# Optimization experiments

Hardware: AMD Instinct MI355X
Metric: run time of the kernel (lower is better)

The kernel has to match this reference:

```python
import jax, jax.numpy as jnp
import numpy as np

B, T, E = 4, 2048, 1024
N, P = 16, 64  # num_heads, projection_dim = E // N
SCALE = P ** 0.5


def setup_inputs() -> dict:
    key = jax.random.key(0)
    k1, k2, k3 = jax.random.split(key, 3)
    x = jax.random.normal(k1, (B, T, E), dtype=jnp.float32)
    w_qkv = jax.random.normal(k2, (E, N, 3 * P), dtype=jnp.float32) * 0.02
    b_qkv = jnp.zeros((N, 3 * P), dtype=jnp.float32)
    w_o = jax.random.normal(k3, (P, N, E), dtype=jnp.float32) * 0.02
    b_o = jnp.zeros((E,), dtype=jnp.float32)
    return {"x": x, "w_qkv": w_qkv, "b_qkv": b_qkv, "w_o": w_o, "b_o": b_o}


def reference(x, w_qkv, b_qkv, w_o, b_o):
    # QKV projection: bte,enp->btnp (+ bias over n,p)
    qkv = jnp.einsum('bte,enp->btnp', x, w_qkv) + b_qkv  # [B,T,N,3P]
    qkv = jnp.transpose(qkv, (0, 2, 1, 3))               # [B,N,T,3P]
    q, k, v = jnp.split(qkv, 3, axis=-1)                 # each [B,N,T,P]
    scores = jnp.einsum('bnip,bnjp->bnij', q, k) / SCALE # [B,N,T,T]
    attn = jax.nn.softmax(scores, axis=-1)
    weighted = jnp.einsum('bnij,bnjp->bnip', attn, v)    # [B,N,T,P]
    # Output projection: bntp,pne->bte (+ bias over e)
    out = jnp.einsum('bntp,pne->bte', weighted, w_o) + b_o
    return out
```

## Files before the change

### kernel.cpp

```cpp
#include <hip/hip_runtime.h>

typedef __attribute__((ext_vector_type(8))) short bf16x8;
typedef __attribute__((ext_vector_type(4))) short s16x4;
typedef __attribute__((ext_vector_type(4))) float f32x4;
typedef __attribute__((ext_vector_type(16))) float f32x16;
typedef __attribute__((ext_vector_type(2))) unsigned u32x2;

#define MFMA16(a,b,c) __builtin_amdgcn_mfma_f32_16x16x32_bf16((a),(b),(c),0,0,0)
#define MFMA32(a,b,c) __builtin_amdgcn_mfma_f32_32x32x16_bf16((a),(b),(c),0,0,0)

static constexpr int Bsz = 4, T = 2048, E = 1024, NH = 16, HP = 64;
static constexpr int J3 = NH * 3 * HP;

__device__ __forceinline__ short f2bf(float f) {
  union { float f; unsigned u; } v; v.f = f;
  unsigned r = (v.u + 0x7fffu + ((v.u >> 16) & 1u)) >> 16;
  return (short)r;
}

__device__ __forceinline__ unsigned cvtpk(float a, float b) {
  unsigned r;
  asm("v_cvt_pk_bf16_f32 %0, %1, %2" : "=v"(r) : "v"(a), "v"(b));
  return r;
}

typedef __attribute__((address_space(3))) unsigned int lds_u32;
typedef __attribute__((address_space(1))) const unsigned int glb_u32;
__device__ __forceinline__ void gl16(const short* g, const short* l) {
  __builtin_amdgcn_global_load_lds((glb_u32*)g, (lds_u32*)l, 16, 0, 0);
}

__global__ void cvt_all(const float* __restrict__ x, s16x4* __restrict__ xb,
                        const float* __restrict__ wqkv, short* __restrict__ wqkvT,
                        const float* __restrict__ wo, short* __restrict__ woT) {
  __shared__ float tile[32][33];
  const int b = blockIdx.x;
  if (b < 8192) {
    int i = b * 256 + threadIdx.x;
    float4 v = ((const float4*)x)[i];
    s16x4 r;
    r[0] = f2bf(v.x); r[1] = f2bf(v.y); r[2] = f2bf(v.z); r[3] = f2bf(v.w);
    xb[i] = r;
  } else if (b < 11264) {
    const int bw = b - 8192;
    const int jb = (bw % 96) * 32, eb = (bw / 96) * 32;
    const int tx = threadIdx.x & 31, ty = threadIdx.x >> 5;
    for (int r = 0; r < 32; r += 8)
      tile[ty + r][tx] = wqkv[(size_t)(eb + ty + r) * J3 + jb + tx];
    __syncthreads();
    for (int r = 0; r < 32; r += 8)
      wqkvT[(size_t)(jb + ty + r) * E + eb + tx] = f2bf(tile[tx][ty + r]);
  } else {
    const int o = (b - 11264) * 256 + threadIdx.x;
    const int e = o >> 10, k = o & 1023;
    const int n = k >> 6, p = k & 63;
    woT[o] = f2bf(wo[(size_t)(p * 16 + n) * E + e]);
  }
}

__global__ __launch_bounds__(256) void gemm_qkv(
    const short* __restrict__ A,
    const short* __restrict__ Bt,
    const float* __restrict__ bias,
    short* __restrict__ Qb, short* __restrict__ Kb, short* __restrict__ Vt) {
  __shared__ short SH[17408];
  short* As = SH;
  short* Bs = SH + 8192;
  const int m0 = blockIdx.x * 128, n0 = blockIdx.y * 128;
  const int tid = threadIdx.x;
  const int lane = tid & 63, w = tid >> 6;
  const int wm = (w >> 1) * 64, wn = (w & 1) * 64;
  const int l15 = lane & 15, lh = lane >> 4;
  const int l7 = l15 & 7;

  const int rA = lane >> 3;
  const int cS = 8 * ((lane & 7) ^ rA);
  const short* Ap = A + (size_t)(m0 + w * 32 + rA) * 1024 + cS;
  const short* Bp = Bt + (size_t)(n0 + w * 32 + rA) * 1024 + cS;
  const short* AsBase = As + w * 2048;
  const short* BsBase = Bs + w * 2048;

  f32x4 acc[4][4] = {};

  for (int k0 = 0; k0 < 1024; k0 += 64) {
    __syncthreads();
#pragma unroll
    for (int j = 0; j < 4; j++) {
      gl16(Ap + j * 8192 + k0, AsBase + j * 512);
      gl16(Bp + j * 8192 + k0, BsBase + j * 512);
    }
    __syncthreads();
    bf16x8 af[2][4], bfr[2][4];
#pragma unroll
    for (int kk = 0; kk < 2; kk++) {
#pragma unroll
      for (int m = 0; m < 4; m++)
        af[kk][m] = *(const bf16x8*)(As + (wm + m * 16 + l15) * 64 + 8 * ((kk * 4 + lh) ^ l7));
#pragma unroll
      for (int n = 0; n < 4; n++)
        bfr[kk][n] = *(const bf16x8*)(Bs + (wn + n * 16 + l15) * 64 + 8 * ((kk * 4 + lh) ^ l7));
    }
#pragma unroll
    for (int m = 0; m < 4; m++)
#pragma unroll
      for (int n = 0; n < 4; n++) {
        acc[m][n] = MFMA16(af[0][m], bfr[0][n], acc[m][n]);
        acc[m][n] = MFMA16(af[1][m], bfr[1][n], acc[m][n]);
      }
  }

  const int bb = m0 >> 11, m0t = m0 & 2047;
  const int g = w & 1;
  const int jg = n0 + g * 64;
  const int nhg = jg / 192;
  const int cg = jg - nhg * 192;
  const int tyg = cg >> 6;

  __syncthreads();
  if (tyg == 2) {
    short* Vl = SH + g * 8704;
#pragma unroll
    for (int nn = 0; nn < 4; nn++) {
      const int p = nn * 16 + l15;
      const float bv = bias[jg + p];
#pragma unroll
      for (int mm = 0; mm < 4; mm++) {
        const int tok0 = wm + mm * 16 + lh * 4;
        u32x2 pk;
        pk[0] = cvtpk(acc[mm][nn][0] + bv, acc[mm][nn][1] + bv);
        pk[1] = cvtpk(acc[mm][nn][2] + bv, acc[mm][nn][3] + bv);
        *(u32x2*)(Vl + p * 136 + tok0) = pk;
      }
    }
  } else {
    const float sc = (tyg == 0) ? 0.180336880f : 1.0f;
    short* qkbase = ((tyg == 0) ? Qb : Kb) +
                    ((((size_t)(bb * 16 + nhg)) * 2048 + m0t) << 6);
#pragma unroll
    for (int nn = 0; nn < 4; nn++) {
      const int p = nn * 16 + l15;
      const float bv = bias[jg + p];
#pragma unroll
      for (int mm = 0; mm < 4; mm++) {
#pragma unroll
        for (int r = 0; r < 4; r++) {
          const int tok = wm + mm * 16 + lh * 4 + r;
          qkbase[(size_t)tok * 64 + p] = f2bf((acc[mm][nn][r] + bv) * sc);
        }
      }
    }
  }
  __syncthreads();
#pragma unroll
  for (int g2 = 0; g2 < 2; g2++) {
    const int jg2 = n0 + g2 * 64;
    const int nh2 = jg2 / 192;
    const int c2 = jg2 - nh2 * 192;
    if ((c2 >> 6) == 2) {
      const short* Vl = SH + g2 * 8704;
      short* vout = Vt + ((size_t)(bb * 16 + nh2) << 6) * 2048 + m0t;
#pragma unroll
      for (int it = 0; it < 4; it++) {
        const int idx = it * 256 + tid;
        const int p = idx >> 4, ch = idx & 15;
        bf16x8 vv = *(const bf16x8*)(Vl + p * 136 + ch * 8);
        *(bf16x8*)(vout + (size_t)p * 2048 + ch * 8) = vv;
      }
    }
  }
}

__global__ __launch_bounds__(512, 4) void attn(
    const short* __restrict__ Qb, const short* __restrict__ Kb,
    const short* __restrict__ Vt, short* __restrict__ Wt) {
  __shared__ short Kl[2][64 * 64];
  __shared__ short Vl[2][64 * 64];
  const int bid = blockIdx.x;
  const int bn = bid & 63, qc = bid >> 6;
  const int tid = threadIdx.x, lane = tid & 63, w = tid >> 6;
  const int l31 = lane & 31, hi = lane >> 5, r7 = l31 & 7;
  const int q0 = qc * 256 + w * 32;

  const short* Qp = Qb + ((size_t)bn * 2048 + q0) * 64;
  const int rA = lane >> 3;
  const int cS = 8 * ((lane & 7) ^ rA);
  const short* Kg = Kb + (size_t)bn * 2048 * 64 + (w * 8 + rA) * 64 + cS;
  const short* Vg = Vt + (size_t)bn * 64 * 2048 + (size_t)(w * 8 + rA) * 2048 + cS;

  bf16x8 qf[4];
#pragma unroll
  for (int kseg = 0; kseg < 4; kseg++)
    qf[kseg] = *(const bf16x8*)(Qp + l31 * 64 + kseg * 16 + hi * 8);

  float l = 0.f;
  f32x16 cin = {};
  f32x16 o0 = {}, o1 = {};

  gl16(Kg, &Kl[0][w * 512]);
  gl16(Vg, &Vl[0][w * 512]);
  __syncthreads();

  for (int t = 0; t < 32; t++) {
    const int cur = t & 1;
    if (t < 31) {
      gl16(Kg + (t + 1) * 4096, &Kl[cur ^ 1][w * 512]);
      gl16(Vg + (t + 1) * 64,   &Vl[cur ^ 1][w * 512]);
    }
    const short* Kc = &Kl[cur][0];
    const short* Vc = &Vl[cur][0];

    f32x16 s0, s1;
    {
      bf16x8 ka = *(const bf16x8*)(Kc + l31 * 64 + 8 * (hi ^ r7));
      s0 = MFMA32(ka, qf[0], cin);
    }
#pragma unroll
    for (int kseg = 1; kseg < 4; kseg++) {
      bf16x8 k0 = *(const bf16x8*)(Kc + l31 * 64 + 8 * ((kseg * 2 + hi) ^ r7));
      s0 = MFMA32(k0, qf[kseg], s0);
    }
    {
      bf16x8 kb = *(const bf16x8*)(Kc + (32 + l31) * 64 + 8 * (hi ^ ((32 + l31) & 7)));
      s1 = MFMA32(kb, qf[0], cin);
    }
#pragma unroll
    for (int kseg = 1; kseg < 4; kseg++) {
      bf16x8 k1 = *(const bf16x8*)(Kc + (32 + l31) * 64 + 8 * ((kseg * 2 + hi) ^ ((32 + l31) & 7)));
      s1 = MFMA32(k1, qf[kseg], s1);
    }

    if (t == 0) {
      float pmax = fmaxf(s0[0], s0[1]);
#pragma unroll
      for (int r = 2; r < 16; r++) pmax = fmaxf(pmax, s0[r]);
#pragma unroll
      for (int r = 0; r < 16; r++) pmax = fmaxf(pmax, s1[r]);
      pmax = fmaxf(pmax, __shfl_xor(pmax, 32, 64));
#pragma unroll
      for (int r = 0; r < 16; r++) {
        s0[r] -= pmax; s1[r] -= pmax; cin[r] = -pmax;
      }
    }

    float p0[16], p1[16], ps = 0.f;
#pragma unroll
    for (int r = 0; r < 16; r++) {
      p0[r] = __builtin_amdgcn_exp2f(s0[r]);
      p1[r] = __builtin_amdgcn_exp2f(s1[r]);
      ps += p0[r] + p1[r];
    }
    ps += __shfl_xor(ps, 32, 64);
    l += ps;

    unsigned wk0[8], wk1[8];
#pragma unroll
    for (int rr = 0; rr < 4; rr++) {
#pragma unroll
      for (int rp = 0; rp < 2; rp++) {
        wk0[rr * 2 + rp] = cvtpk(p0[rr * 4 + 2 * rp], p0[rr * 4 + 2 * rp + 1]);
        wk1[rr * 2 + rp] = cvtpk(p1[rr * 4 + 2 * rp], p1[rr * 4 + 2 * rp + 1]);
      }
    }
    union U8 { unsigned u[4]; bf16x8 v; };
    bf16x8 pb[4];
#pragma unroll
    for (int kseg = 0; kseg < 4; kseg++) {
      const int rrA = 2 * (kseg & 1);
      U8 u;
#pragma unroll
      for (int rp = 0; rp < 2; rp++) {
        unsigned a = (kseg < 2) ? wk0[rrA * 2 + rp] : wk1[rrA * 2 + rp];
        unsigned b = (kseg < 2) ? wk0[(rrA + 1) * 2 + rp] : wk1[(rrA + 1) * 2 + rp];
        asm("v_permlane32_swap_b32 %0, %1" : "+v"(a), "+v"(b));
        u.u[rp] = a;
        u.u[2 + rp] = b;
      }
      pb[kseg] = u.v;
    }

#pragma unroll
    for (int kseg = 0; kseg < 4; kseg++) {
      bf16x8 v0 = *(const bf16x8*)(Vc + l31 * 64 + 8 * ((kseg * 2 + hi) ^ r7));
      o0 = MFMA32(v0, pb[kseg], o0);
    }
#pragma unroll
    for (int kseg = 0; kseg < 4; kseg++) {
      bf16x8 v1 = *(const bf16x8*)(Vc + (32 + l31) * 64 + 8 * ((kseg * 2 + hi) ^ ((32 + l31) & 7)));
      o1 = MFMA32(v1, pb[kseg], o1);
    }
    __syncthreads();
  }

  const float invl = 1.0f / l;
  const int bb = bn >> 4, n = bn & 15;
  short* wrow = Wt + (size_t)(bb * 2048 + q0 + l31) * 1024 + n * 64;
#pragma unroll
  for (int rr = 0; rr < 4; rr++) {
    s16x4 pk0, pk1;
#pragma unroll
    for (int j = 0; j < 4; j++) {
      pk0[j] = f2bf(o0[rr * 4 + j] * invl);
      pk1[j] = f2bf(o1[rr * 4 + j] * invl);
    }
    *(s16x4*)(wrow + 8 * rr + 4 * hi) = pk0;
    *(s16x4*)(wrow + 32 + 8 * rr + 4 * hi) = pk1;
  }
}

__global__ __launch_bounds__(256) void gemm_o(
    const short* __restrict__ A,
    const short* __restrict__ Bt,
    const float* __restrict__ bo,
    float* __restrict__ out) {
  __shared__ short As[128 * 64];
  __shared__ short Bs[128 * 64];
  const int m0 = blockIdx.x * 128, n0 = blockIdx.y * 128;
  const int tid = threadIdx.x;
  const int lane = tid & 63, w = tid >> 6;
  const int wm = (w >> 1) * 64, wn = (w & 1) * 64;
  const int l15 = lane & 15, lh = lane >> 4;
  const int l7 = l15 & 7;

  const int rA = lane >> 3;
  const int cS = 8 * ((lane & 7) ^ rA);
  const short* Ap = A + (size_t)(m0 + w * 32 + rA) * 1024 + cS;
  const short* Bp = Bt + (size_t)(n0 + w * 32 + rA) * 1024 + cS;
  const short* AsBase = As + w * 2048;
  const short* BsBase = Bs + w * 2048;

  f32x4 acc[4][4] = {};

  for (int k0 = 0; k0 < 1024; k0 += 64) {
    __syncthreads();
#pragma unroll
    for (int j = 0; j < 4; j++) {
      gl16(Ap + j * 8192 + k0, AsBase + j * 512);
      gl16(Bp + j * 8192 + k0, BsBase + j * 512);
    }
    __syncthreads();
    bf16x8 af[2][4], bfr[2][4];
#pragma unroll
    for (int kk = 0; kk < 2; kk++) {
#pragma unroll
      for (int m = 0; m < 4; m++)
        af[kk][m] = *(const bf16x8*)(As + (wm + m * 16 + l15) * 64 + 8 * ((kk * 4 + lh) ^ l7));
#pragma unroll
      for (int n = 0; n < 4; n++)
        bfr[kk][n] = *(const bf16x8*)(Bs + (wn + n * 16 + l15) * 64 + 8 * ((kk * 4 + lh) ^ l7));
    }
#pragma unroll
    for (int m = 0; m < 4; m++)
#pragma unroll
      for (int n = 0; n < 4; n++) {
        acc[m][n] = MFMA16(af[0][m], bfr[0][n], acc[m][n]);
        acc[m][n] = MFMA16(af[1][m], bfr[1][n], acc[m][n]);
      }
  }

#pragma unroll
  for (int nn = 0; nn < 4; nn++) {
    int e = n0 + wn + nn * 16 + l15;
    float bv = bo[e];
#pragma unroll
    for (int mm = 0; mm < 4; mm++) {
#pragma unroll
      for (int r = 0; r < 4; r++) {
        int i = m0 + wm + mm * 16 + lh * 4 + r;
        out[(size_t)i * 1024 + e] = acc[mm][nn][r] + bv;
      }
    }
  }
}

extern "C" void kernel_launch(void* const* d_in, const int* in_sizes, int n_in,
                              void* d_out, int out_size, void* d_ws, size_t ws_size,
                              hipStream_t stream) {
  (void)in_sizes; (void)n_in; (void)out_size; (void)ws_size;
  const float* x     = (const float*)d_in[0];
  const float* w_qkv = (const float*)d_in[1];
  const float* b_qkv = (const float*)d_in[2];
  const float* w_o   = (const float*)d_in[3];
  const float* b_o   = (const float*)d_in[4];
  float* out = (float*)d_out;
  char* ws = (char*)d_ws;

  short* xb     = (short*)(ws);
  short* wqkvbT = (short*)(ws + 16777216);
  short* wobT   = (short*)(ws + 23068672);
  short* Qb     = (short*)(ws + 25165824);
  short* Kb     = (short*)(ws + 41943040);
  short* Vt     = (short*)(ws + 58720256);
  short* Wt     = (short*)(ws + 75497472);

  hipLaunchKernelGGL(cvt_all,  dim3(15360),   dim3(256), 0, stream,
                     x, (s16x4*)xb, w_qkv, wqkvbT, w_o, wobT);
  hipLaunchKernelGGL(gemm_qkv, dim3(64, 24),  dim3(256), 0, stream, xb, wqkvbT, b_qkv, Qb, Kb, Vt);
  hipLaunchKernelGGL(attn,     dim3(512),     dim3(512), 0, stream, Qb, Kb, Vt, Wt);
  hipLaunchKernelGGL(gemm_o,   dim3(64, 8),   dim3(256), 0, stream, Wt, wobT, b_o, out);
}
```

Before: 169.2 us.

## Process two 32-row query tiles per wave in attention to reuse K/V fragments

Each attention wave now handles 64 query rows (two 32-row sub-tiles) instead of 32, and the block shrinks from 512 to 256 threads while covering the same 256 queries. Each V fragment read from LDS now feeds two MFMAs, and each thread issues twice as many async K/V loads per tile. The goal is to cut LDS read traffic per MFMA and barrier overhead per unit of work. The cost is roughly double the accumulator and register state per wave, which lowers occupancy (launch bounds 256,2) and may cause spills.

```diff
diff --git a/kernel.cpp b/kernel.cpp
--- a/kernel.cpp
+++ b/kernel.cpp
@@ -170,7 +170,7 @@
   }
 }
 
-__global__ __launch_bounds__(512, 4) void attn(
+__global__ __launch_bounds__(256, 2) void attn(
     const short* __restrict__ Qb, const short* __restrict__ Kb,
     const short* __restrict__ Vt, short* __restrict__ Wt) {
   __shared__ short Kl[2][64 * 64];
@@ -179,131 +179,217 @@
   const int bn = bid & 63, qc = bid >> 6;
   const int tid = threadIdx.x, lane = tid & 63, w = tid >> 6;
   const int l31 = lane & 31, hi = lane >> 5, r7 = l31 & 7;
-  const int q0 = qc * 256 + w * 32;
+  const int q0 = qc * 256 + w * 64;
 
   const short* Qp = Qb + ((size_t)bn * 2048 + q0) * 64;
   const int rA = lane >> 3;
-  const int cS = 8 * ((lane & 7) ^ rA);
-  const short* Kg = Kb + (size_t)bn * 2048 * 64 + (w * 8 + rA) * 64 + cS;
-  const short* Vg = Vt + (size_t)bn * 64 * 2048 + (size_t)(w * 8 + rA) * 2048 + cS;
-
-  bf16x8 qf[4];
-#pragma unroll
-  for (int kseg = 0; kseg < 4; kseg++)
-    qf[kseg] = *(const bf16x8*)(Qp + l31 * 64 + kseg * 16 + hi * 8);
-
-  float l = 0.f;
-  f32x16 cin = {};
-  f32x16 o0 = {}, o1 = {};
-
-  gl16(Kg, &Kl[0][w * 512]);
-  gl16(Vg, &Vl[0][w * 512]);
+  const int cSw = 8 * ((lane & 7) ^ rA);
+  const short* Kg = Kb + (size_t)bn * 2048 * 64 + (w * 16 + rA) * 64 + cSw;
+  const short* Vg = Vt + (size_t)bn * 64 * 2048 + (size_t)(w * 16 + rA) * 2048 + cSw;
+
+  bf16x8 qfA[4], qfB[4];
+#pragma unroll
+  for (int kseg = 0; kseg < 4; kseg++) {
+    qfA[kseg] = *(const bf16x8*)(Qp + l31 * 64 + kseg * 16 + hi * 8);
+    qfB[kseg] = *(const bf16x8*)(Qp + (32 + l31) * 64 + kseg * 16 + hi * 8);
+  }
+
+  float lA = 0.f, lB = 0.f;
+  f32x16 cinA = {}, cinB = {};
+  f32x16 oA0 = {}, oA1 = {}, oB0 = {}, oB1 = {};
+
+  gl16(Kg,         &Kl[0][w * 1024]);
+  gl16(Kg + 512,   &Kl[0][w * 1024 + 512]);
+  gl16(Vg,         &Vl[0][w * 1024]);
+  gl16(Vg + 16384, &Vl[0][w * 1024 + 512]);
   __syncthreads();
+
+  union U8 { unsigned u[4]; bf16x8 v; };
 
   for (int t = 0; t < 32; t++) {
     const int cur = t & 1;
     if (t < 31) {
-      gl16(Kg + (t + 1) * 4096, &Kl[cur ^ 1][w * 512]);
-      gl16(Vg + (t + 1) * 64,   &Vl[cur ^ 1][w * 512]);
+      const short* kg = Kg + (t + 1) * 4096;
+      const short* vg = Vg + (t + 1) * 64;
+      gl16(kg,         &Kl[cur ^ 1][w * 1024]);
+      gl16(kg + 512,   &Kl[cur ^ 1][w * 1024 + 512]);
+      gl16(vg,         &Vl[cur ^ 1][w * 1024]);
+      gl16(vg + 16384, &Vl[cur ^ 1][w * 1024 + 512]);
     }
     const short* Kc = &Kl[cur][0];
     const short* Vc = &Vl[cur][0];
 
-    f32x16 s0, s1;
+    bf16x8 pbA[4], pbB[4];
+
     {
-      bf16x8 ka = *(const bf16x8*)(Kc + l31 * 64 + 8 * (hi ^ r7));
-      s0 = MFMA32(ka, qf[0], cin);
-    }
-#pragma unroll
-    for (int kseg = 1; kseg < 4; kseg++) {
-      bf16x8 k0 = *(const bf16x8*)(Kc + l31 * 64 + 8 * ((kseg * 2 + hi) ^ r7));
-      s0 = MFMA32(k0, qf[kseg], s0);
+      f32x16 s0, s1;
+      {
+        bf16x8 ka = *(const bf16x8*)(Kc + l31 * 64 + 8 * (hi ^ r7));
+        s0 = MFMA32(ka, qfA[0], cinA);
+      }
+#pragma unroll
+      for (int kseg = 1; kseg < 4; kseg++) {
+        bf16x8 k0 = *(const bf16x8*)(Kc + l31 * 64 + 8 * ((kseg * 2 + hi) ^ r7));
+        s0 = MFMA32(k0, qfA[kseg], s0);
+      }
+      {
+        bf16x8 kb = *(const bf16x8*)(Kc + (32 + l31) * 64 + 8 * (hi ^ r7));
+        s1 = MFMA32(kb, qfA[0], cinA);
+      }
+#pragma unroll
+      for (int kseg = 1; kseg < 4; kseg++) {
+        bf16x8 k1 = *(const bf16x8*)(Kc + (32 + l31) * 64 + 8 * ((kseg * 2 + hi) ^ r7));
+        s1 = MFMA32(k1, qfA[kseg], s1);
+      }
+      if (t == 0) {
+        float pmax = fmaxf(s0[0], s0[1]);
+#pragma unroll
+        for (int r = 2; r < 16; r++) pmax = fmaxf(pmax, s0[r]);
+#pragma unroll
+        for (int r = 0; r < 16; r++) pmax = fmaxf(pmax, s1[r]);
+        pmax = fmaxf(pmax, __shfl_xor(pmax, 32, 64));
+#pragma unroll
+        for (int r = 0; r < 16; r++) { s0[r] -= pmax; s1[r] -= pmax; cinA[r] = -pmax; }
+      }
+      float p0[16], p1[16], ps = 0.f;
+#pragma unroll
+      for (int r = 0; r < 16; r++) {
+        p0[r] = __builtin_amdgcn_exp2f(s0[r]);
+        p1[r] = __builtin_amdgcn_exp2f(s1[r]);
+        ps += p0[r] + p1[r];
+      }
+      ps += __shfl_xor(ps, 32, 64);
+      lA += ps;
+      unsigned wk0[8], wk1[8];
+#pragma unroll
+      for (int rr = 0; rr < 4; rr++)
+#pragma unroll
+        for (int rp = 0; rp < 2; rp++) {
+          wk0[rr * 2 + rp] = cvtpk(p0[rr * 4 + 2 * rp], p0[rr * 4 + 2 * rp + 1]);
+          wk1[rr * 2 + rp] = cvtpk(p1[rr * 4 + 2 * rp], p1[rr * 4 + 2 * rp + 1]);
+        }
+#pragma unroll
+      for (int kseg = 0; kseg < 4; kseg++) {
+        const int rr2 = 2 * (kseg & 1);
+        U8 u;
+#pragma unroll
+        for (int rp = 0; rp < 2; rp++) {
+          unsigned a = (kseg < 2) ? wk0[rr2 * 2 + rp] : wk1[rr2 * 2 + rp];
+          unsigned b = (kseg < 2) ? wk0[(rr2 + 1) * 2 + rp] : wk1[(rr2 + 1) * 2 + rp];
+          asm("v_permlane32_swap_b32 %0, %1" : "+v"(a), "+v"(b));
+          u.u[rp] = a;
+          u.u[2 + rp] = b;
+        }
+        pbA[kseg] = u.v;
+      }
     }
     {
-      bf16x8 kb = *(const bf16x8*)(Kc + (32 + l31) * 64 + 8 * (hi ^ ((32 + l31) & 7)));
-      s1 = MFMA32(kb, qf[0], cin);
-    }
-#pragma unroll
-    for (int kseg = 1; kseg < 4; kseg++) {
-      bf16x8 k1 = *(const bf16x8*)(Kc + (32 + l31) * 64 + 8 * ((kseg * 2 + hi) ^ ((32 + l31) & 7)));
-      s1 = MFMA32(k1, qf[kseg], s1);
-    }
-
-    if (t == 0) {
-      float pmax = fmaxf(s0[0], s0[1]);
-#pragma unroll
-      for (int r = 2; r < 16; r++) pmax = fmaxf(pmax, s0[r]);
-#pragma unroll
-      for (int r = 0; r < 16; r++) pmax = fmaxf(pmax, s1[r]);
-      pmax = fmaxf(pmax, __shfl_xor(pmax, 32, 64));
+      f32x16 s0, s1;
+      {
+        bf16x8 ka = *(const bf16x8*)(Kc + l31 * 64 + 8 * (hi ^ r7));
+        s0 = MFMA32(ka, qfB[0], cinB);
+      }
+#pragma unroll
+      for (int kseg = 1; kseg < 4; kseg++) {
+        bf16x8 k0 = *(const bf16x8*)(Kc + l31 * 64 + 8 * ((kseg * 2 + hi) ^ r7));
+        s0 = MFMA32(k0, qfB[kseg], s0);
+      }
+      {
+        bf16x8 kb = *(const bf16x8*)(Kc + (32 + l31) * 64 + 8 * (hi ^ r7));
+        s1 = MFMA32(kb, qfB[0], cinB);
+      }
+#pragma unroll
+      for (int kseg = 1; kseg < 4; kseg++) {
+        bf16x8 k1 = *(const bf16x8*)(Kc + (32 + l31) * 64 + 8 * ((kseg * 2 + hi) ^ r7));
+        s1 = MFMA32(k1, qfB[kseg], s1);
+      }
+      if (t == 0) {
+        float pmax = fmaxf(s0[0], s0[1]);
+#pragma unroll
+        for (int r = 2; r < 16; r++) pmax = fmaxf(pmax, s0[r]);
+#pragma unroll
+        for (int r = 0; r < 16; r++) pmax = fmaxf(pmax, s1[r]);
+        pmax = fmaxf(pmax, __shfl_xor(pmax, 32, 64));
+#pragma unroll
+        for (int r = 0; r < 16; r++) { s0[r] -= pmax; s1[r] -= pmax; cinB[r] = -pmax; }
+      }
+      float p0[16], p1[16], ps = 0.f;
 #pragma unroll
       for (int r = 0; r < 16; r++) {
-        s0[r] -= pmax; s1[r] -= pmax; cin[r] = -pmax;
-      }
-    }
-
-    float p0[16], p1[16], ps = 0.f;
-#pragma unroll
-    for (int r = 0; r < 16; r++) {
-      p0[r] = __builtin_amdgcn_exp2f(s0[r]);
-      p1[r] = __builtin_amdgcn_exp2f(s1[r]);
-      ps += p0[r] + p1[r];
-    }
-    ps += __shfl_xor(ps, 32, 64);
-    l += ps;
-
-    unsigned wk0[8], wk1[8];
-#pragma unroll
-    for (int rr = 0; rr < 4; rr++) {
-#pragma unroll
-      for (int rp = 0; rp < 2; rp++) {
-        wk0[rr * 2 + rp] = cvtpk(p0[rr * 4 + 2 * rp], p0[rr * 4 + 2 * rp + 1]);
-        wk1[rr * 2 + rp] = cvtpk(p1[rr * 4 + 2 * rp], p1[rr * 4 + 2 * rp + 1]);
-      }
-    }
-    union U8 { unsigned u[4]; bf16x8 v; };
-    bf16x8 pb[4];
-#pragma unroll
-    for (int kseg = 0; kseg < 4; kseg++) {
-      const int rrA = 2 * (kseg & 1);
-      U8 u;
-#pragma unroll
-      for (int rp = 0; rp < 2; rp++) {
-        unsigned a = (kseg < 2) ? wk0[rrA * 2 + rp] : wk1[rrA * 2 + rp];
-        unsigned b = (kseg < 2) ? wk0[(rrA + 1) * 2 + rp] : wk1[(rrA + 1) * 2 + rp];
-        asm("v_permlane32_swap_b32 %0, %1" : "+v"(a), "+v"(b));
-        u.u[rp] = a;
-        u.u[2 + rp] = b;
-      }
-      pb[kseg] = u.v;
-    }
-
+        p0[r] = __builtin_amdgcn_exp2f(s0[r]);
+        p1[r] = __builtin_amdgcn_exp2f(s1[r]);
+        ps += p0[r] + p1[r];
+      }
+      ps += __shfl_xor(ps, 32, 64);
+      lB += ps;
+      unsigned wk0[8], wk1[8];
+#pragma unroll
+      for (int rr = 0; rr < 4; rr++)
+#pragma unroll
+        for (int rp = 0; rp < 2; rp++) {
+          wk0[rr * 2 + rp] = cvtpk(p0[rr * 4 + 2 * rp], p0[rr * 4 + 2 * rp + 1]);
+          wk1[rr * 2 + rp] = cvtpk(p1[rr * 4 + 2 * rp], p1[rr * 4 + 2 * rp + 1]);
+        }
+#pragma unroll
+      for (int kseg = 0; kseg < 4; kseg++) {
+        const int rr2 = 2 * (kseg & 1);
+        U8 u;
+#pragma unroll
+        for (int rp = 0; rp < 2; rp++) {
+          unsigned a = (kseg < 2) ? wk0[rr2 * 2 + rp] : wk1[rr2 * 2 + rp];
+          unsigned b = (kseg < 2) ? wk0[(rr2 + 1) * 2 + rp] : wk1[(rr2 + 1) * 2 + rp];
+          asm("v_permlane32_swap_b32 %0, %1" : "+v"(a), "+v"(b));
+          u.u[rp] = a;
+          u.u[2 + rp] = b;
+        }
+        pbB[kseg] = u.v;
+      }
+    }
 #pragma unroll
     for (int kseg = 0; kseg < 4; kseg++) {
       bf16x8 v0 = *(const bf16x8*)(Vc + l31 * 64 + 8 * ((kseg * 2 + hi) ^ r7));
-      o0 = MFMA32(v0, pb[kseg], o0);
+      oA0 = MFMA32(v0, pbA[kseg], oA0);
+      oB0 = MFMA32(v0, pbB[kseg], oB0);
     }
 #pragma unroll
     for (int kseg = 0; kseg < 4; kseg++) {
-      bf16x8 v1 = *(const bf16x8*)(Vc + (32 + l31) * 64 + 8 * ((kseg * 2 + hi) ^ ((32 + l31) & 7)));
-      o1 = MFMA32(v1, pb[kseg], o1);
-    }
-    __syncthreads();
-  }
-
-  const float invl = 1.0f / l;
+      bf16x8 v1 = *(const bf16x8*)(Vc + (32 + l31) * 64 + 8 * ((kseg * 2 + hi) ^ r7));
+      oA1 = MFMA32(v1, pbA[kseg], oA1);
+      oB1 = MFMA32(v1, pbB[kseg], oB1);
+    }
+    __syncthreads();
+  }
+
   const int bb = bn >> 4, n = bn & 15;
-  short* wrow = Wt + (size_t)(bb * 2048 + q0 + l31) * 1024 + n * 64;
-#pragma unroll
-  for (int rr = 0; rr < 4; rr++) {
-    s16x4 pk0, pk1;
-#pragma unroll
-    for (int j = 0; j < 4; j++) {
-      pk0[j] = f2bf(o0[rr * 4 + j] * invl);
-      pk1[j] = f2bf(o1[rr * 4 + j] * invl);
-    }
-    *(s16x4*)(wrow + 8 * rr + 4 * hi) = pk0;
-    *(s16x4*)(wrow + 32 + 8 * rr + 4 * hi) = pk1;
+  {
+    const float invl = 1.0f / lA;
+    short* wrow = Wt + (size_t)(bb * 2048 + q0 + l31) * 1024 + n * 64;
+#pragma unroll
+    for (int rr = 0; rr < 4; rr++) {
+      s16x4 pk0, pk1;
+#pragma unroll
+      for (int j = 0; j < 4; j++) {
+        pk0[j] = f2bf(oA0[rr * 4 + j] * invl);
+        pk1[j] = f2bf(oA1[rr * 4 + j] * invl);
+      }
+      *(s16x4*)(wrow + 8 * rr + 4 * hi) = pk0;
+      *(s16x4*)(wrow + 32 + 8 * rr + 4 * hi) = pk1;
+    }
+  }
+  {
+    const float invl = 1.0f / lB;
+    short* wrow = Wt + (size_t)(bb * 2048 + q0 + 32 + l31) * 1024 + n * 64;
+#pragma unroll
+    for (int rr = 0; rr < 4; rr++) {
+      s16x4 pk0, pk1;
+#pragma unroll
+      for (int j = 0; j < 4; j++) {
+        pk0[j] = f2bf(oB0[rr * 4 + j] * invl);
+        pk1[j] = f2bf(oB1[rr * 4 + j] * invl);
+      }
+      *(s16x4*)(wrow + 8 * rr + 4 * hi) = pk0;
+      *(s16x4*)(wrow + 32 + 8 * rr + 4 * hi) = pk1;
+    }
   }
 }
 
@@ -395,6 +481,6 @@
   hipLaunchKernelGGL(cvt_all,  dim3(15360),   dim3(256), 0, stream,
                      x, (s16x4*)xb, w_qkv, wqkvbT, w_o, wobT);
   hipLaunchKernelGGL(gemm_qkv, dim3(64, 24),  dim3(256), 0, stream, xb, wqkvbT, b_qkv, Qb, Kb, Vt);
-  hipLaunchKernelGGL(attn,     dim3(512),     dim3(512), 0, stream, Qb, Kb, Vt, Wt);
+  hipLaunchKernelGGL(attn,     dim3(512),     dim3(256), 0, stream, Qb, Kb, Vt, Wt);
   hipLaunchKernelGGL(gemm_o,   dim3(64, 8),   dim3(256), 0, stream, Wt, wobT, b_o, out);
 }
```

Result: slower. 175.0 us (+3.4%).
